# Kernel tuning notes

Hardware: AMD Instinct MI355X
Metric: run time of the kernel (lower is better)

Reference implementation:

```python
import jax, jax.numpy as jnp
import numpy as np
import math

NH = 12
EPS = 1e-7
BUCKET = 32
MAX_POS = 512

def make_position_indices(seq_len=MAX_POS, bucket_size=BUCKET, max_position=MAX_POS):
    rel = np.arange(max_position)[:, None] - np.arange(max_position)[None, :]
    sign = np.sign(rel)
    mid = bucket_size // 2
    abs_pos = np.where((rel < mid) & (rel > -mid), mid - 1, np.abs(rel)).astype(np.float64)
    log_pos = np.ceil(np.log(abs_pos / mid) / math.log((max_position - 1) / mid) * (mid - 1)).astype(np.int64) + mid
    bucket_pos = np.where(abs_pos <= mid, rel, log_pos * sign).astype(np.int64)
    idx = (bucket_size - 1 + bucket_pos).astype(np.int32)
    return idx[:seq_len, :seq_len]

def setup_inputs() -> dict:
    key = jax.random.key(0)
    S, B, H, I, L = 512, 8, 768, 2048, 6
    ks = jax.random.split(key, 16)
    std = math.sqrt(2.0 / (5.0 * H))
    inp = {
        'hidden_states': jax.random.normal(ks[0], (S, B, H), jnp.float32),
        'attention_mask': jnp.zeros((B, 1, 1, S), dtype=bool),
        'relative_embedding': jax.random.normal(ks[1], (2 * BUCKET - 1, H), jnp.float32) * 0.02,
        'Wqk': jax.random.normal(ks[2], (L, 2 * H, H), jnp.float32) * std,
        'bqk': jnp.zeros((L, 2 * H), jnp.float32),
        'Wv': jax.random.normal(ks[3], (L, H, H), jnp.float32) * std,
        'bv': jnp.zeros((L, H), jnp.float32),
        'Wo': jax.random.normal(ks[4], (L, H, H), jnp.float32) * std,
        'bo': jnp.zeros((L, H), jnp.float32),
        'ln_g': jnp.ones((L, H), jnp.float32),
        'ln_b': jnp.zeros((L, H), jnp.float32),
        'W1': jax.random.normal(ks[5], (L, 2 * I, H), jnp.float32) * std,
        'W2': jax.random.normal(ks[6], (L, H, I), jnp.float32) * std,
        'position_indices': jnp.asarray(make_position_indices(S)),
    }
    return inp

def _ln(x):
    mu = jnp.mean(x, axis=-1, keepdims=True)
    xc = x - mu
    var = jnp.mean(xc * xc, axis=-1, keepdims=True)
    return xc / jnp.sqrt(var + EPS)

def _encoder(hidden_states, attention_mask, relative_embedding, Wqk, bqk, Wv, bv, Wo, bo, ln_g, ln_b, W1, W2, position_indices):
    S, B, H = hidden_states.shape
    hd = H // NH
    scale = 1.0 / math.sqrt(3 * hd)
    mask = attention_mask  # bool [B,1,1,S], True = masked out

    def layer(x, p):
        Wqk_, bqk_, Wv_, bv_, Wo_, bo_, g_, b_, W1_, W2_ = p
        h = _ln(x)  # pre-LN, no affine
        qk = h @ Wqk_.T + bqk_            # [S,B,2H]
        q, k = jnp.split(qk, 2, axis=-1)
        v = h @ Wv_.T + bv_               # [S,B,H]
        # relative position projections
        pos = relative_embedding @ Wqk_.T + bqk_          # [R,2H]
        pos = pos[position_indices]                        # [S,S,2H]
        pos = pos.reshape(S, S, NH, 2 * hd)
        qpos, kpos = pos[..., :hd], pos[..., hd:]          # [S,S,NH,hd]
        q = q.reshape(S, B, NH, hd).transpose(1, 2, 0, 3)  # [B,NH,S,hd]
        k = k.reshape(S, B, NH, hd).transpose(1, 2, 0, 3)
        v = v.reshape(S, B, NH, hd).transpose(1, 2, 0, 3)
        scores = jnp.einsum('bhqd,bhkd->bhqk', q, k) * scale
        scores = scores + jnp.einsum('bhqd,qkhd->bhqk', q, kpos) * scale
        scores = scores + jnp.einsum('bhkd,qkhd->bhqk', k, qpos) * scale
        scores = jnp.where(mask, -jnp.inf, scores)
        probs = jax.nn.softmax(scores, axis=-1)
        probs = jnp.where(mask, 0.0, probs)
        ctx = jnp.einsum('bhqk,bhkd->bhqd', probs, v)      # [B,NH,S,hd]
        ctx = ctx.transpose(2, 0, 1, 3).reshape(S, B, H)
        ctx = ctx @ Wo_.T + bo_
        ctx = _ln(ctx) * g_ + b_                            # post-LN with affine
        x = x + ctx
        # GeGLU FFN
        h = _ln(x)
        u = h @ W1_.T                                       # [S,B,2I]
        a, gate = jnp.split(u, 2, axis=-1)
        u = a * jax.nn.gelu(gate, approximate=True)
        u = _ln(u)
        u = u @ W2_.T
        x = x + u
        return x, None

    x, _ = jax.lax.scan(layer, hidden_states, (Wqk, bqk, Wv, bv, Wo, bo, ln_g, ln_b, W1, W2))
    return x

def reference(hidden_states, attention_mask, relative_embedding, Wqk, bqk, Wv, bv, Wo, bo, ln_g, ln_b, W1, W2, position_indices):
    return _encoder(hidden_states, attention_mask, relative_embedding, Wqk, bqk, Wv, bv, Wo, bo, ln_g, ln_b, W1, W2, position_indices)
```

## Files before the change

### kernel.cpp

```cpp
#include <hip/hip_runtime.h>
#include <math.h>

typedef unsigned short u16;
typedef unsigned int u32;
typedef short bf16x8 __attribute__((ext_vector_type(8)));
typedef float f32x4 __attribute__((ext_vector_type(4)));

__device__ __forceinline__ float bf2f(u16 b) {
    u32 x = ((u32)b) << 16;
    return __builtin_bit_cast(float, x);
}
__device__ __forceinline__ u16 f2bf(float f) {
    u32 u = __builtin_bit_cast(u32, f);
    u32 r = (u + 0x7fffu + ((u >> 16) & 1u)) >> 16;
    return (u16)r;
}
__device__ __forceinline__ float wave_red_sum(float v) {
#pragma unroll
    for (int o = 32; o; o >>= 1) v += __shfl_down(v, o, 64);
    return v;
}


__global__ void convert_kernel(const float* __restrict__ in, u16* __restrict__ out, int n) {
    for (int i = blockIdx.x * 256 + threadIdx.x; i < n; i += gridDim.x * 256)
        out[i] = f2bf(in[i]);
}

__global__ void copy_kernel(const float* __restrict__ in, float* __restrict__ out, int n) {
    for (int i = blockIdx.x * 256 + threadIdx.x; i < n; i += gridDim.x * 256)
        out[i] = in[i];
}

__global__ void relpad_kernel(const float* __restrict__ rel, u16* __restrict__ relpad) {
    int i = blockIdx.x * 256 + threadIdx.x;
    if (i >= 64 * 768) return;
    relpad[i] = (i < 63 * 768) ? f2bf(rel[i]) : (u16)0;
}

__global__ void diag_kernel(unsigned char* __restrict__ diag8) {
    int i = blockIdx.x * 256 + threadIdx.x;
    if (i >= 1023) return;
    int rel = i - 511;
    int sgn = (rel > 0) - (rel < 0);
    int arel = rel < 0 ? -rel : rel;
    double abs_pos = (rel < 16 && rel > -16) ? 15.0 : (double)arel;
    int bucket;
    if (abs_pos <= 16.0) {
        bucket = rel;
    } else {
        double lp = ceil(log(abs_pos / 16.0) / log(511.0 / 16.0) * 15.0);
        bucket = ((int)lp + 16) * sgn;
    }
    diag8[i] = (unsigned char)(31 + bucket);
}

__global__ __launch_bounds__(256) void ln_plain(const float* __restrict__ x, u16* __restrict__ h) {
    int m = blockIdx.x, t = threadIdx.x;
    const float* row = x + (size_t)m * 768;
    float v0 = row[t], v1 = row[t + 256], v2 = row[t + 512];
    __shared__ float red[4];
    float s = wave_red_sum(v0 + v1 + v2);
    if ((t & 63) == 0) red[t >> 6] = s;
    __syncthreads();
    float mean = (red[0] + red[1] + red[2] + red[3]) * (1.f / 768.f);
    __syncthreads();
    float d0 = v0 - mean, d1 = v1 - mean, d2 = v2 - mean;
    float q = wave_red_sum(d0 * d0 + d1 * d1 + d2 * d2);
    if ((t & 63) == 0) red[t >> 6] = q;
    __syncthreads();
    float inv = rsqrtf((red[0] + red[1] + red[2] + red[3]) * (1.f / 768.f) + 1e-7f);
    u16* hr = h + (size_t)m * 768;
    hr[t] = f2bf(d0 * inv);
    hr[t + 256] = f2bf(d1 * inv);
    hr[t + 512] = f2bf(d2 * inv);
}

__global__ __launch_bounds__(256) void ln_res(const float* __restrict__ c, const float* __restrict__ g,
                                              const float* __restrict__ bb, float* __restrict__ x) {
    int m = blockIdx.x, t = threadIdx.x;
    const float* row = c + (size_t)m * 768;
    float v0 = row[t], v1 = row[t + 256], v2 = row[t + 512];
    __shared__ float red[4];
    float s = wave_red_sum(v0 + v1 + v2);
    if ((t & 63) == 0) red[t >> 6] = s;
    __syncthreads();
    float mean = (red[0] + red[1] + red[2] + red[3]) * (1.f / 768.f);
    __syncthreads();
    float d0 = v0 - mean, d1 = v1 - mean, d2 = v2 - mean;
    float q = wave_red_sum(d0 * d0 + d1 * d1 + d2 * d2);
    if ((t & 63) == 0) red[t >> 6] = q;
    __syncthreads();
    float inv = rsqrtf((red[0] + red[1] + red[2] + red[3]) * (1.f / 768.f) + 1e-7f);
    float* xr = x + (size_t)m * 768;
    xr[t] += d0 * inv * g[t] + bb[t];
    xr[t + 256] += d1 * inv * g[t + 256] + bb[t + 256];
    xr[t + 512] += d2 * inv * g[t + 512] + bb[t + 512];
}

__device__ __forceinline__ float fast_tanh(float z) {
    return 1.f - 2.f / (__expf(2.f * z) + 1.f);
}

__global__ __launch_bounds__(256) void glu_ln(const u16* __restrict__ u, u16* __restrict__ h2) {
    int m = blockIdx.x, t = threadIdx.x;
    const u16* row = u + (size_t)m * 4096;
    float gv[8];
    float s = 0.f;
#pragma unroll
    for (int jj = 0; jj < 8; jj++) {
        int j = jj * 256 + t;
        float a = bf2f(row[j]);
        float gt = bf2f(row[2048 + j]);
        float ge = 0.5f * gt * (1.f + fast_tanh(0.7978845608028654f * (gt + 0.044715f * gt * gt * gt)));
        gv[jj] = a * ge;
        s += gv[jj];
    }
    __shared__ float red[4];
    s = wave_red_sum(s);
    if ((t & 63) == 0) red[t >> 6] = s;
    __syncthreads();
    float mean = (red[0] + red[1] + red[2] + red[3]) * (1.f / 2048.f);
    __syncthreads();
    float q2 = 0.f;
#pragma unroll
    for (int jj = 0; jj < 8; jj++) {
        float d = gv[jj] - mean;
        q2 += d * d;
    }
    q2 = wave_red_sum(q2);
    if ((t & 63) == 0) red[t >> 6] = q2;
    __syncthreads();
    float inv = rsqrtf((red[0] + red[1] + red[2] + red[3]) * (1.f / 2048.f) + 1e-7f);
    u16* out = h2 + (size_t)m * 2048;
#pragma unroll
    for (int jj = 0; jj < 8; jj++) out[jj * 256 + t] = f2bf((gv[jj] - mean) * inv);
}

__global__ __launch_bounds__(256) void gemm_nt(const u16* __restrict__ A, const u16* __restrict__ B,
                                               const float* __restrict__ bias, int M, int N, int K,
                                               int mode, void* __restrict__ out0, void* __restrict__ out1) {
    __shared__ __align__(16) u16 As[128 * 72];
    __shared__ __align__(16) u16 Bs[128 * 72];
    const int t = threadIdx.x;
    const int lane = t & 63, wave = t >> 6;
    const int wm = (wave >> 1) * 64, wn = (wave & 1) * 64;
    const int fr = lane & 15, qd = lane >> 4;
    const int m0 = blockIdx.y * 128, n0 = blockIdx.x * 128;
    const int row_s = t >> 3, g_s = t & 7;

    f32x4 zero4 = {0.f, 0.f, 0.f, 0.f};
    f32x4 acc[4][4];
#pragma unroll
    for (int i = 0; i < 4; i++)
#pragma unroll
        for (int j = 0; j < 4; j++) acc[i][j] = zero4;

    for (int k0 = 0; k0 < K; k0 += 64) {
        __syncthreads();
#pragma unroll
        for (int it = 0; it < 4; ++it) {
            int row = it * 32 + row_s;
            const float4* src = (const float4*)(A + (size_t)(m0 + row) * K + k0 + g_s * 8);
            *(float4*)&As[row * 72 + g_s * 8] = *src;
        }
#pragma unroll
        for (int it = 0; it < 4; ++it) {
            int row = it * 32 + row_s;
            const float4* src = (const float4*)(B + (size_t)(n0 + row) * K + k0 + g_s * 8);
            *(float4*)&Bs[row * 72 + g_s * 8] = *src;
        }
        __syncthreads();
#pragma unroll
        for (int s = 0; s < 2; ++s) {
            bf16x8 aF[4], bF[4];
#pragma unroll
            for (int i = 0; i < 4; i++) aF[i] = *(const bf16x8*)&As[(wm + i * 16 + fr) * 72 + s * 32 + qd * 8];
#pragma unroll
            for (int j = 0; j < 4; j++) bF[j] = *(const bf16x8*)&Bs[(wn + j * 16 + fr) * 72 + s * 32 + qd * 8];
#pragma unroll
            for (int i = 0; i < 4; i++)
#pragma unroll
                for (int j = 0; j < 4; j++)
                    acc[i][j] = __builtin_amdgcn_mfma_f32_16x16x32_bf16(aF[i], bF[j], acc[i][j], 0, 0, 0);
        }
    }

#pragma unroll
    for (int j = 0; j < 4; j++) {
        int nn = n0 + wn + j * 16 + fr;
        float bval = bias ? bias[nn] : 0.f;
#pragma unroll
        for (int i = 0; i < 4; i++) {
#pragma unroll
            for (int rg = 0; rg < 4; ++rg) {
                int mm = m0 + wm + i * 16 + qd * 4 + rg;
                float val = acc[i][j][rg] + bval;
                if (mode == 0) {
                    ((float*)out0)[(size_t)mm * N + nn] = val;
                } else if (mode == 1) {
                    ((u16*)out0)[(size_t)mm * N + nn] = f2bf(val);
                } else if (mode == 2) {
                    int sidx = mm >> 3, bidx = mm & 7;
                    int nn2 = nn;
                    u16* dst = (u16*)out0;
                    if (nn2 >= 768) { dst = (u16*)out1; nn2 -= 768; }
                    int hh = nn2 >> 6, dd = nn2 & 63;
                    dst[(size_t)((bidx * 12 + hh) * 512 + sidx) * 64 + dd] = f2bf(val);
                } else if (mode == 3) {
                    int sidx = mm >> 3, bidx = mm & 7;
                    int hh = nn >> 6, dd = nn & 63;
                    ((u16*)out0)[(size_t)((bidx * 12 + hh) * 64 + dd) * 512 + sidx] = f2bf(val);
                } else {
                    ((float*)out0)[(size_t)mm * N + nn] += val;
                }
            }
        }
    }
}


__global__ __launch_bounds__(256) void pos_mfma(const u16* __restrict__ relpad, const u16* __restrict__ wqk_all,
                                                const float* __restrict__ bqk_all, u16* __restrict__ qposb,
                                                u16* __restrict__ kposb) {
    __shared__ __align__(16) u16 As[64 * 72];
    __shared__ __align__(16) u16 Bs[64 * 72];
    int t = threadIdx.x, lane = t & 63, w = t >> 6;
    int fr = lane & 15, qd = lane >> 4;
    int n0 = blockIdx.x * 64, l = blockIdx.y;
    const u16* B = wqk_all + (size_t)l * 1536 * 768;
    const float* bias = bqk_all + (size_t)l * 1536;
    int rs = t >> 2, cs = (t & 3) * 16;
    f32x4 zero4 = {0.f, 0.f, 0.f, 0.f};
    f32x4 acc[4];
#pragma unroll
    for (int j = 0; j < 4; j++) acc[j] = zero4;

    for (int k0 = 0; k0 < 768; k0 += 64) {
        __syncthreads();
        const u16* ga = relpad + (size_t)rs * 768 + k0 + cs;
        *(float4*)&As[rs * 72 + cs] = *(const float4*)ga;
        *(float4*)&As[rs * 72 + cs + 8] = *(const float4*)(ga + 8);
        const u16* gb = B + (size_t)(n0 + rs) * 768 + k0 + cs;
        *(float4*)&Bs[rs * 72 + cs] = *(const float4*)gb;
        *(float4*)&Bs[rs * 72 + cs + 8] = *(const float4*)(gb + 8);
        __syncthreads();
#pragma unroll
        for (int s = 0; s < 2; s++) {
            bf16x8 aF = *(const bf16x8*)&As[(w * 16 + fr) * 72 + s * 32 + qd * 8];
#pragma unroll
            for (int jf = 0; jf < 4; jf++) {
                bf16x8 bF = *(const bf16x8*)&Bs[(jf * 16 + fr) * 72 + s * 32 + qd * 8];
                acc[jf] = __builtin_amdgcn_mfma_f32_16x16x32_bf16(aF, bF, acc[jf], 0, 0, 0);
            }
        }
    }
#pragma unroll
    for (int jf = 0; jf < 4; jf++) {
        int nn = n0 + jf * 16 + fr;
        float bval = bias[nn];
        int hh = nn >> 7, wd = nn & 127;
#pragma unroll
        for (int rg = 0; rg < 4; rg++) {
            int m = w * 16 + qd * 4 + rg;
            if (m >= 63) continue;
            float val = acc[jf][rg] + bval;
            size_t o = ((size_t)l * 12 + hh) * 64 * 64 + (size_t)m * 64;
            if (wd < 64) qposb[o + wd] = f2bf(val);
            else kposb[o + (wd - 64)] = f2bf(val);
        }
    }
}

__global__ __launch_bounds__(256) void posdot_kernel(const u16* __restrict__ qbuf, const u16* __restrict__ kbuf,
                                                     const u16* __restrict__ qposb, const u16* __restrict__ kposb,
                                                     u16* __restrict__ c2pb, u16* __restrict__ p2cb) {
    __shared__ __align__(16) u16 Qs[128 * 72];
    __shared__ __align__(16) u16 Ks[128 * 72];
    __shared__ __align__(16) u16 QP[64 * 72];
    __shared__ __align__(16) u16 KP[64 * 72];
    const float scale = 0.07216878364870323f;
    int t = threadIdx.x, lane = t & 63, w = t >> 6;
    int fr = lane & 15, qd = lane >> 4;
    int s0 = blockIdx.x * 128, bh = blockIdx.y, h = bh % 12;
    size_t base = (size_t)bh * 512 * 64;
    {
        int rs = t >> 1, cs = (t & 1) * 32;
#pragma unroll
        for (int c = 0; c < 4; c++) {
            *(float4*)&Qs[rs * 72 + cs + c * 8] = *(const float4*)(qbuf + base + (size_t)(s0 + rs) * 64 + cs + c * 8);
            *(float4*)&Ks[rs * 72 + cs + c * 8] = *(const float4*)(kbuf + base + (size_t)(s0 + rs) * 64 + cs + c * 8);
        }
        int rs2 = t >> 2, cs2 = (t & 3) * 16;
        const u16* qp = qposb + (size_t)h * 64 * 64;
        const u16* kp = kposb + (size_t)h * 64 * 64;
#pragma unroll
        for (int c = 0; c < 2; c++) {
            *(float4*)&QP[rs2 * 72 + cs2 + c * 8] = *(const float4*)(qp + (size_t)rs2 * 64 + cs2 + c * 8);
            *(float4*)&KP[rs2 * 72 + cs2 + c * 8] = *(const float4*)(kp + (size_t)rs2 * 64 + cs2 + c * 8);
        }
    }
    __syncthreads();
    f32x4 zero4 = {0.f, 0.f, 0.f, 0.f};
    f32x4 cacc[2][4], pacc[2][4];
#pragma unroll
    for (int i = 0; i < 2; i++)
#pragma unroll
        for (int j = 0; j < 4; j++) { cacc[i][j] = zero4; pacc[i][j] = zero4; }
#pragma unroll
    for (int s = 0; s < 2; s++) {
#pragma unroll
        for (int i = 0; i < 2; i++) {
            bf16x8 aQ = *(const bf16x8*)&Qs[(w * 32 + i * 16 + fr) * 72 + s * 32 + qd * 8];
            bf16x8 aK = *(const bf16x8*)&Ks[(w * 32 + i * 16 + fr) * 72 + s * 32 + qd * 8];
#pragma unroll
            for (int jf = 0; jf < 4; jf++) {
                bf16x8 bKP = *(const bf16x8*)&KP[(jf * 16 + fr) * 72 + s * 32 + qd * 8];
                bf16x8 bQP = *(const bf16x8*)&QP[(jf * 16 + fr) * 72 + s * 32 + qd * 8];
                cacc[i][jf] = __builtin_amdgcn_mfma_f32_16x16x32_bf16(aQ, bKP, cacc[i][jf], 0, 0, 0);
                pacc[i][jf] = __builtin_amdgcn_mfma_f32_16x16x32_bf16(aK, bQP, pacc[i][jf], 0, 0, 0);
            }
        }
    }
#pragma unroll
    for (int i = 0; i < 2; i++)
#pragma unroll
        for (int jf = 0; jf < 4; jf++)
#pragma unroll
            for (int rg = 0; rg < 4; rg++) {
                int row = w * 32 + i * 16 + qd * 4 + rg;
                int col = jf * 16 + fr;
                size_t o = (size_t)(bh * 512 + s0 + row) * 64 + col;
                c2pb[o] = f2bf(cacc[i][jf][rg] * scale);
                p2cb[o] = f2bf(pacc[i][jf][rg] * scale);
            }
}

__global__ __launch_bounds__(256) void attn_mfma(const u16* __restrict__ qbuf, const u16* __restrict__ kbuf,
                                                 const u16* __restrict__ vbT, const u16* __restrict__ c2pb,
                                                 const u16* __restrict__ p2cb, const unsigned char* __restrict__ diag8,
                                                 const unsigned char* __restrict__ mask, u16* __restrict__ ctxb) {
    __shared__ __align__(16) u16 Qs[64 * 72];
    __shared__ __align__(16) u16 KsPs[64 * 72];
    __shared__ __align__(16) u16 Vt[64 * 72];
    __shared__ __align__(16) u16 c2ps[64 * 72];
    __shared__ __align__(16) u16 p2cs[64 * 72];
    __shared__ unsigned char idxd[576];
    __shared__ unsigned char mks[512];
    const float scale = 0.07216878364870323f;
    int t = threadIdx.x, lane = t & 63, w = t >> 6;
    int fr = lane & 15, qd = lane >> 4;
    int qt = blockIdx.x, bh = blockIdx.y;
    int b = bh / 12, h = bh % 12;
    int q0 = qt * 64;
    size_t base = (size_t)bh * 512 * 64;
    int rs = t >> 2, cs = (t & 3) * 16;

    {
        const u16* gq = qbuf + base + (size_t)(q0 + rs) * 64 + cs;
        *(float4*)&Qs[rs * 72 + cs] = *(const float4*)gq;
        *(float4*)&Qs[rs * 72 + cs + 8] = *(const float4*)(gq + 8);
        const u16* gc = c2pb + (size_t)(bh * 512 + q0 + rs) * 64 + cs;
        *(float4*)&c2ps[rs * 72 + cs] = *(const float4*)gc;
        *(float4*)&c2ps[rs * 72 + cs + 8] = *(const float4*)(gc + 8);
        for (int i = t; i < 575; i += 256) idxd[i] = diag8[q0 + i];
        for (int i = t; i < 512; i += 256) mks[i] = mask[b * 512 + i];
    }

    f32x4 zero4 = {0.f, 0.f, 0.f, 0.f};
    f32x4 oacc[4];
#pragma unroll
    for (int j = 0; j < 4; j++) oacc[j] = zero4;
    float m_i[4] = {-1e30f, -1e30f, -1e30f, -1e30f};
    float l_i[4] = {0.f, 0.f, 0.f, 0.f};
    const int ql0 = w * 16 + qd * 4;

    for (int kt = 0; kt < 8; kt++) {
        __syncthreads();
        {
            const u16* gk = kbuf + base + (size_t)(kt * 64 + rs) * 64 + cs;
            *(float4*)&KsPs[rs * 72 + cs] = *(const float4*)gk;
            *(float4*)&KsPs[rs * 72 + cs + 8] = *(const float4*)(gk + 8);
            const u16* gv = vbT + base + (size_t)rs * 512 + kt * 64 + cs;
            *(float4*)&Vt[rs * 72 + cs] = *(const float4*)gv;
            *(float4*)&Vt[rs * 72 + cs + 8] = *(const float4*)(gv + 8);
            const u16* gp = p2cb + (size_t)(bh * 512 + kt * 64 + rs) * 64 + cs;
            *(float4*)&p2cs[rs * 72 + cs] = *(const float4*)gp;
            *(float4*)&p2cs[rs * 72 + cs + 8] = *(const float4*)(gp + 8);
        }
        __syncthreads();

        f32x4 sacc[4];
#pragma unroll
        for (int j = 0; j < 4; j++) sacc[j] = zero4;
#pragma unroll
        for (int s = 0; s < 2; s++) {
            bf16x8 aQ = *(const bf16x8*)&Qs[(w * 16 + fr) * 72 + s * 32 + qd * 8];
#pragma unroll
            for (int jf = 0; jf < 4; jf++) {
                bf16x8 bK = *(const bf16x8*)&KsPs[(jf * 16 + fr) * 72 + s * 32 + qd * 8];
                sacc[jf] = __builtin_amdgcn_mfma_f32_16x16x32_bf16(aQ, bK, sacc[jf], 0, 0, 0);
            }
        }

        float pvv[4][4];
#pragma unroll
        for (int jf = 0; jf < 4; jf++) {
            int kl = jf * 16 + fr;
            int kg = kt * 64 + kl;
            bool mk = mks[kg] != 0;
#pragma unroll
            for (int rg = 0; rg < 4; rg++) {
                int ql = ql0 + rg;
                int j = idxd[ql - kg + 511];
                float bias = bf2f(c2ps[ql * 72 + j]) + bf2f(p2cs[kl * 72 + j]);
                float sval = sacc[jf][rg] * scale + bias;
                pvv[jf][rg] = mk ? -1e30f : sval;
            }
        }

#pragma unroll
        for (int rg = 0; rg < 4; rg++) {
            float rm = fmaxf(fmaxf(pvv[0][rg], pvv[1][rg]), fmaxf(pvv[2][rg], pvv[3][rg]));
#pragma unroll
            for (int msk = 1; msk < 16; msk <<= 1) rm = fmaxf(rm, __shfl_xor(rm, msk));
            float mnew = fmaxf(m_i[rg], rm);
            float alpha = __expf(m_i[rg] - mnew);
            m_i[rg] = mnew;
            float rsum = 0.f;
#pragma unroll
            for (int jf = 0; jf < 4; jf++) {
                float p = __expf(pvv[jf][rg] - mnew);
                pvv[jf][rg] = p;
                rsum += p;
            }
#pragma unroll
            for (int msk = 1; msk < 16; msk <<= 1) rsum += __shfl_xor(rsum, msk);
            l_i[rg] = l_i[rg] * alpha + rsum;
#pragma unroll
            for (int jf = 0; jf < 4; jf++) oacc[jf][rg] *= alpha;
        }

        __syncthreads();

        u16* Psw = &KsPs[w * 16 * 72];
#pragma unroll
        for (int jf = 0; jf < 4; jf++)
#pragma unroll
            for (int rg = 0; rg < 4; rg++) Psw[(qd * 4 + rg) * 72 + jf * 16 + fr] = f2bf(pvv[jf][rg]);

#pragma unroll
        for (int s = 0; s < 2; s++) {
            bf16x8 aP = *(const bf16x8*)&Psw[fr * 72 + s * 32 + qd * 8];
#pragma unroll
            for (int jf = 0; jf < 4; jf++) {
                bf16x8 bV = *(const bf16x8*)&Vt[(jf * 16 + fr) * 72 + s * 32 + qd * 8];
                oacc[jf] = __builtin_amdgcn_mfma_f32_16x16x32_bf16(aP, bV, oacc[jf], 0, 0, 0);
            }
        }
    }

#pragma unroll
    for (int jf = 0; jf < 4; jf++) {
#pragma unroll
        for (int rg = 0; rg < 4; rg++) {
            int qg = q0 + ql0 + rg;
            int d = jf * 16 + fr;
            float o = oacc[jf][rg] / l_i[rg];
            int m = qg * 8 + b;
            ctxb[(size_t)m * 768 + h * 64 + d] = f2bf(o);
        }
    }
}


extern "C" void kernel_launch(void* const* d_in, const int* in_sizes, int n_in, void* d_out, int out_size,
                              void* d_ws, size_t ws_size, hipStream_t stream) {
    const float* hidden = (const float*)d_in[0];
    const unsigned char* mask = (const unsigned char*)d_in[1];
    const float* relemb = (const float*)d_in[2];
    const float* Wqk = (const float*)d_in[3];
    const float* bqk = (const float*)d_in[4];
    const float* Wv = (const float*)d_in[5];
    const float* bv = (const float*)d_in[6];
    const float* Wo = (const float*)d_in[7];
    const float* bo = (const float*)d_in[8];
    const float* lng = (const float*)d_in[9];
    const float* lnb = (const float*)d_in[10];
    const float* W1 = (const float*)d_in[11];
    const float* W2 = (const float*)d_in[12];
    float* x = (float*)d_out;

    char* wsp = (char*)d_ws;
    auto alloc = [&](size_t bytes) -> char* {
        char* p = wsp;
        wsp += (bytes + 255) & ~(size_t)255;
        return p;
    };
    u16* wqk_bf = (u16*)alloc(6ull * 1536 * 768 * 2);
    u16* wv_bf = (u16*)alloc(6ull * 768 * 768 * 2);
    u16* wo_bf = (u16*)alloc(6ull * 768 * 768 * 2);
    u16* w1_bf = (u16*)alloc(6ull * 4096 * 768 * 2);
    u16* w2_bf = (u16*)alloc(6ull * 768 * 2048 * 2);
    u16* h_bf = (u16*)alloc(4096ull * 768 * 2);
    u16* qb = (u16*)alloc(96ull * 512 * 64 * 2);
    u16* kb = (u16*)alloc(96ull * 512 * 64 * 2);
    u16* vbT = (u16*)alloc(96ull * 512 * 64 * 2);
    u16* qposb = (u16*)alloc(6ull * 12 * 64 * 64 * 2);
    u16* kposb = (u16*)alloc(6ull * 12 * 64 * 64 * 2);
    u16* relpad = (u16*)alloc(64ull * 768 * 2);
    u16* c2pb = (u16*)alloc(96ull * 512 * 64 * 2);
    u16* p2cb = (u16*)alloc(96ull * 512 * 64 * 2);
    unsigned char* diag8 = (unsigned char*)alloc(1024);
    u16* ctxb = (u16*)alloc(4096ull * 768 * 2);
    float* ctxproj = (float*)alloc(4096ull * 768 * 4);
    u16* ubuf = (u16*)alloc(4096ull * 4096 * 2);
    u16* h2 = (u16*)alloc(4096ull * 2048 * 2);
    (void)ws_size;
    (void)in_sizes;
    (void)n_in;
    (void)out_size;

    auto conv = [&](const float* in, u16* out, size_t n) {
        size_t blocks = (n + 255) / 256;
        if (blocks > 8192) blocks = 8192;
        convert_kernel<<<dim3((unsigned)blocks), dim3(256), 0, stream>>>(in, out, (int)n);
    };
    conv(Wqk, wqk_bf, 6ull * 1536 * 768);
    conv(Wv, wv_bf, 6ull * 768 * 768);
    conv(Wo, wo_bf, 6ull * 768 * 768);
    conv(W1, w1_bf, 6ull * 4096 * 768);
    conv(W2, w2_bf, 6ull * 768 * 2048);
    copy_kernel<<<dim3(4096), dim3(256), 0, stream>>>(hidden, x, 4096 * 768);
    diag_kernel<<<dim3(4), dim3(256), 0, stream>>>(diag8);
    relpad_kernel<<<dim3(192), dim3(256), 0, stream>>>(relemb, relpad);
    pos_mfma<<<dim3(24, 6), dim3(256), 0, stream>>>(relpad, wqk_bf, bqk, qposb, kposb);

    for (int l = 0; l < 6; l++) {
        ln_plain<<<dim3(4096), dim3(256), 0, stream>>>(x, h_bf);
        gemm_nt<<<dim3(12, 32), dim3(256), 0, stream>>>(h_bf, wqk_bf + (size_t)l * 1536 * 768, bqk + l * 1536,
                                                        4096, 1536, 768, 2, qb, kb);
        gemm_nt<<<dim3(6, 32), dim3(256), 0, stream>>>(h_bf, wv_bf + (size_t)l * 768 * 768, bv + l * 768,
                                                       4096, 768, 768, 3, vbT, nullptr);
        posdot_kernel<<<dim3(4, 96), dim3(256), 0, stream>>>(qb, kb, qposb + (size_t)l * 12 * 64 * 64,
                                                             kposb + (size_t)l * 12 * 64 * 64, c2pb, p2cb);
        attn_mfma<<<dim3(8, 96), dim3(256), 0, stream>>>(qb, kb, vbT, c2pb, p2cb, diag8, mask, ctxb);
        gemm_nt<<<dim3(6, 32), dim3(256), 0, stream>>>(ctxb, wo_bf + (size_t)l * 768 * 768, bo + l * 768,
                                                       4096, 768, 768, 0, ctxproj, nullptr);
        ln_res<<<dim3(4096), dim3(256), 0, stream>>>(ctxproj, lng + l * 768, lnb + l * 768, x);
        ln_plain<<<dim3(4096), dim3(256), 0, stream>>>(x, h_bf);
        gemm_nt<<<dim3(32, 32), dim3(256), 0, stream>>>(h_bf, w1_bf + (size_t)l * 4096 * 768, nullptr,
                                                        4096, 4096, 768, 1, ubuf, nullptr);
        glu_ln<<<dim3(4096), dim3(256), 0, stream>>>(ubuf, h2);
        gemm_nt<<<dim3(6, 32), dim3(256), 0, stream>>>(h2, w2_bf + (size_t)l * 768 * 2048, nullptr,
                                                       4096, 768, 2048, 4, x, nullptr);
    }
}
```

Measured before the change: 1.861 ms.

## Fuse QKV projection GEMMs and use 64x64 tiles for narrow N=768 GEMMs

The Wqk and Wv weights and biases are concatenated into one [2304,768] matrix per layer, so the Q/K and V projections run as a single GEMM whose epilogue scatters into the q, k and transposed v layouts. The output-projection and FFN down-projection GEMMs (N=768) move to a new 64x64-tile kernel with a grid of 768 blocks instead of 192, which fills more compute units on the device, plus an XCD-aware block-index remap. The smaller tiles give less data reuse per block, and the fused epilogue adds a branch per element.

Measured after the change: 1.658 ms. -10.9%, faster.

```diff
diff --git a/kernel.cpp b/kernel.cpp
--- a/kernel.cpp
+++ b/kernel.cpp
@@ -25,6 +25,26 @@
 __global__ void convert_kernel(const float* __restrict__ in, u16* __restrict__ out, int n) {
     for (int i = blockIdx.x * 256 + threadIdx.x; i < n; i += gridDim.x * 256)
         out[i] = f2bf(in[i]);
+}
+
+__global__ void convert_qkv_kernel(const float* __restrict__ Wqk, const float* __restrict__ Wv,
+                                   u16* __restrict__ out) {
+    const int per = 2304 * 768;
+    for (int i = blockIdx.x * 256 + threadIdx.x; i < 6 * per; i += gridDim.x * 256) {
+        int l = i / per, r = i % per;
+        int row = r / 768, col = r % 768;
+        float v = (row < 1536) ? Wqk[((size_t)l * 1536 + row) * 768 + col]
+                               : Wv[((size_t)l * 768 + (row - 1536)) * 768 + col];
+        out[i] = f2bf(v);
+    }
+}
+
+__global__ void bias_qkv_kernel(const float* __restrict__ bqk, const float* __restrict__ bv,
+                                float* __restrict__ out) {
+    for (int i = blockIdx.x * 256 + threadIdx.x; i < 6 * 2304; i += gridDim.x * 256) {
+        int l = i / 2304, r = i % 2304;
+        out[i] = (r < 1536) ? bqk[l * 1536 + r] : bv[l * 768 + (r - 1536)];
+    }
 }
 
 __global__ void copy_kernel(const float* __restrict__ in, float* __restrict__ out, int n) {
@@ -139,7 +159,8 @@
 
 __global__ __launch_bounds__(256) void gemm_nt(const u16* __restrict__ A, const u16* __restrict__ B,
                                                const float* __restrict__ bias, int M, int N, int K,
-                                               int mode, void* __restrict__ out0, void* __restrict__ out1) {
+                                               int mode, void* __restrict__ out0, void* __restrict__ out1,
+                                               void* __restrict__ out2) {
     __shared__ __align__(16) u16 As[128 * 72];
     __shared__ __align__(16) u16 Bs[128 * 72];
     const int t = threadIdx.x;
@@ -196,40 +217,106 @@
             for (int rg = 0; rg < 4; ++rg) {
                 int mm = m0 + wm + i * 16 + qd * 4 + rg;
                 float val = acc[i][j][rg] + bval;
-                if (mode == 0) {
-                    ((float*)out0)[(size_t)mm * N + nn] = val;
-                } else if (mode == 1) {
+                if (mode == 1) {
                     ((u16*)out0)[(size_t)mm * N + nn] = f2bf(val);
-                } else if (mode == 2) {
+                } else {
                     int sidx = mm >> 3, bidx = mm & 7;
-                    int nn2 = nn;
-                    u16* dst = (u16*)out0;
-                    if (nn2 >= 768) { dst = (u16*)out1; nn2 -= 768; }
-                    int hh = nn2 >> 6, dd = nn2 & 63;
-                    dst[(size_t)((bidx * 12 + hh) * 512 + sidx) * 64 + dd] = f2bf(val);
-                } else if (mode == 3) {
-                    int sidx = mm >> 3, bidx = mm & 7;
-                    int hh = nn >> 6, dd = nn & 63;
-                    ((u16*)out0)[(size_t)((bidx * 12 + hh) * 64 + dd) * 512 + sidx] = f2bf(val);
-                } else {
-                    ((float*)out0)[(size_t)mm * N + nn] += val;
+                    if (nn < 1536) {
+                        int nn2 = nn;
+                        u16* dst = (u16*)out0;
+                        if (nn2 >= 768) { dst = (u16*)out1; nn2 -= 768; }
+                        int hh = nn2 >> 6, dd = nn2 & 63;
+                        dst[(size_t)((bidx * 12 + hh) * 512 + sidx) * 64 + dd] = f2bf(val);
+                    } else {
+                        int nn2 = nn - 1536;
+                        int hh = nn2 >> 6, dd = nn2 & 63;
+                        ((u16*)out2)[(size_t)((bidx * 12 + hh) * 64 + dd) * 512 + sidx] = f2bf(val);
+                    }
                 }
             }
         }
     }
 }
 
-
-__global__ __launch_bounds__(256) void pos_mfma(const u16* __restrict__ relpad, const u16* __restrict__ wqk_all,
-                                                const float* __restrict__ bqk_all, u16* __restrict__ qposb,
+__global__ __launch_bounds__(256) void gemm64(const u16* __restrict__ A, const u16* __restrict__ B,
+                                              const float* __restrict__ bias, int M, int N, int K,
+                                              int mode, float* __restrict__ out) {
+    __shared__ __align__(16) u16 As[64 * 72];
+    __shared__ __align__(16) u16 Bs[64 * 72];
+    const int t = threadIdx.x;
+    const int lane = t & 63, w = t >> 6;
+    const int wm = (w >> 1) * 32, wn = (w & 1) * 32;
+    const int fr = lane & 15, qd = lane >> 4;
+    const int nt = N >> 6, mt = M >> 6;
+    int lin = blockIdx.x;
+    int c = lin & 7, s = lin >> 3;
+    int m0 = (c * (mt >> 3) + s / nt) * 64;
+    int n0 = (s % nt) * 64;
+    const int rs = t >> 2, cs = (t & 3) * 16;
+
+    f32x4 zero4 = {0.f, 0.f, 0.f, 0.f};
+    f32x4 acc[2][2];
+#pragma unroll
+    for (int i = 0; i < 2; i++)
+#pragma unroll
+        for (int j = 0; j < 2; j++) acc[i][j] = zero4;
+
+    for (int k0 = 0; k0 < K; k0 += 64) {
+        __syncthreads();
+        {
+            const u16* ga = A + (size_t)(m0 + rs) * K + k0 + cs;
+            *(float4*)&As[rs * 72 + cs] = *(const float4*)ga;
+            *(float4*)&As[rs * 72 + cs + 8] = *(const float4*)(ga + 8);
+            const u16* gb = B + (size_t)(n0 + rs) * K + k0 + cs;
+            *(float4*)&Bs[rs * 72 + cs] = *(const float4*)gb;
+            *(float4*)&Bs[rs * 72 + cs + 8] = *(const float4*)(gb + 8);
+        }
+        __syncthreads();
+#pragma unroll
+        for (int s2 = 0; s2 < 2; ++s2) {
+            bf16x8 aF[2], bF[2];
+#pragma unroll
+            for (int i = 0; i < 2; i++) aF[i] = *(const bf16x8*)&As[(wm + i * 16 + fr) * 72 + s2 * 32 + qd * 8];
+#pragma unroll
+            for (int j = 0; j < 2; j++) bF[j] = *(const bf16x8*)&Bs[(wn + j * 16 + fr) * 72 + s2 * 32 + qd * 8];
+#pragma unroll
+            for (int i = 0; i < 2; i++)
+#pragma unroll
+                for (int j = 0; j < 2; j++)
+                    acc[i][j] = __builtin_amdgcn_mfma_f32_16x16x32_bf16(aF[i], bF[j], acc[i][j], 0, 0, 0);
+        }
+    }
+
+#pragma unroll
+    for (int j = 0; j < 2; j++) {
+        int nn = n0 + wn + j * 16 + fr;
+        float bval = bias ? bias[nn] : 0.f;
+#pragma unroll
+        for (int i = 0; i < 2; i++) {
+#pragma unroll
+            for (int rg = 0; rg < 4; ++rg) {
+                int mm = m0 + wm + i * 16 + qd * 4 + rg;
+                float val = acc[i][j][rg] + bval;
+                if (mode == 0)
+                    out[(size_t)mm * N + nn] = val;
+                else
+                    out[(size_t)mm * N + nn] += val;
+            }
+        }
+    }
+}
+
+
+__global__ __launch_bounds__(256) void pos_mfma(const u16* __restrict__ relpad, const u16* __restrict__ wqkv_all,
+                                                const float* __restrict__ bqkv_all, u16* __restrict__ qposb,
                                                 u16* __restrict__ kposb) {
     __shared__ __align__(16) u16 As[64 * 72];
     __shared__ __align__(16) u16 Bs[64 * 72];
     int t = threadIdx.x, lane = t & 63, w = t >> 6;
     int fr = lane & 15, qd = lane >> 4;
     int n0 = blockIdx.x * 64, l = blockIdx.y;
-    const u16* B = wqk_all + (size_t)l * 1536 * 768;
-    const float* bias = bqk_all + (size_t)l * 1536;
+    const u16* B = wqkv_all + (size_t)l * 2304 * 768;
+    const float* bias = bqkv_all + (size_t)l * 2304;
     int rs = t >> 2, cs = (t & 3) * 16;
     f32x4 zero4 = {0.f, 0.f, 0.f, 0.f};
     f32x4 acc[4];
@@ -497,8 +584,8 @@
         wsp += (bytes + 255) & ~(size_t)255;
         return p;
     };
-    u16* wqk_bf = (u16*)alloc(6ull * 1536 * 768 * 2);
-    u16* wv_bf = (u16*)alloc(6ull * 768 * 768 * 2);
+    u16* wqkv_bf = (u16*)alloc(6ull * 2304 * 768 * 2);
+    float* bqkv = (float*)alloc(6ull * 2304 * 4);
     u16* wo_bf = (u16*)alloc(6ull * 768 * 768 * 2);
     u16* w1_bf = (u16*)alloc(6ull * 4096 * 768 * 2);
     u16* w2_bf = (u16*)alloc(6ull * 768 * 2048 * 2);
@@ -526,33 +613,31 @@
         if (blocks > 8192) blocks = 8192;
         convert_kernel<<<dim3((unsigned)blocks), dim3(256), 0, stream>>>(in, out, (int)n);
     };
-    conv(Wqk, wqk_bf, 6ull * 1536 * 768);
-    conv(Wv, wv_bf, 6ull * 768 * 768);
+    convert_qkv_kernel<<<dim3(8192), dim3(256), 0, stream>>>(Wqk, Wv, wqkv_bf);
+    bias_qkv_kernel<<<dim3(54), dim3(256), 0, stream>>>(bqk, bv, bqkv);
     conv(Wo, wo_bf, 6ull * 768 * 768);
     conv(W1, w1_bf, 6ull * 4096 * 768);
     conv(W2, w2_bf, 6ull * 768 * 2048);
     copy_kernel<<<dim3(4096), dim3(256), 0, stream>>>(hidden, x, 4096 * 768);
     diag_kernel<<<dim3(4), dim3(256), 0, stream>>>(diag8);
     relpad_kernel<<<dim3(192), dim3(256), 0, stream>>>(relemb, relpad);
-    pos_mfma<<<dim3(24, 6), dim3(256), 0, stream>>>(relpad, wqk_bf, bqk, qposb, kposb);
+    pos_mfma<<<dim3(24, 6), dim3(256), 0, stream>>>(relpad, wqkv_bf, bqkv, qposb, kposb);
 
     for (int l = 0; l < 6; l++) {
         ln_plain<<<dim3(4096), dim3(256), 0, stream>>>(x, h_bf);
-        gemm_nt<<<dim3(12, 32), dim3(256), 0, stream>>>(h_bf, wqk_bf + (size_t)l * 1536 * 768, bqk + l * 1536,
-                                                        4096, 1536, 768, 2, qb, kb);
-        gemm_nt<<<dim3(6, 32), dim3(256), 0, stream>>>(h_bf, wv_bf + (size_t)l * 768 * 768, bv + l * 768,
-                                                       4096, 768, 768, 3, vbT, nullptr);
+        gemm_nt<<<dim3(18, 32), dim3(256), 0, stream>>>(h_bf, wqkv_bf + (size_t)l * 2304 * 768, bqkv + l * 2304,
+                                                        4096, 2304, 768, 5, qb, kb, vbT);
         posdot_kernel<<<dim3(4, 96), dim3(256), 0, stream>>>(qb, kb, qposb + (size_t)l * 12 * 64 * 64,
                                                              kposb + (size_t)l * 12 * 64 * 64, c2pb, p2cb);
         attn_mfma<<<dim3(8, 96), dim3(256), 0, stream>>>(qb, kb, vbT, c2pb, p2cb, diag8, mask, ctxb);
-        gemm_nt<<<dim3(6, 32), dim3(256), 0, stream>>>(ctxb, wo_bf + (size_t)l * 768 * 768, bo + l * 768,
-                                                       4096, 768, 768, 0, ctxproj, nullptr);
+        gemm64<<<dim3(768), dim3(256), 0, stream>>>(ctxb, wo_bf + (size_t)l * 768 * 768, bo + l * 768,
+                                                    4096, 768, 768, 0, ctxproj);
         ln_res<<<dim3(4096), dim3(256), 0, stream>>>(ctxproj, lng + l * 768, lnb + l * 768, x);
         ln_plain<<<dim3(4096), dim3(256), 0, stream>>>(x, h_bf);
         gemm_nt<<<dim3(32, 32), dim3(256), 0, stream>>>(h_bf, w1_bf + (size_t)l * 4096 * 768, nullptr,
-                                                        4096, 4096, 768, 1, ubuf, nullptr);
+                                                        4096, 4096, 768, 1, ubuf, nullptr, nullptr);
         glu_ln<<<dim3(4096), dim3(256), 0, stream>>>(ubuf, h2);
-        gemm_nt<<<dim3(6, 32), dim3(256), 0, stream>>>(h2, w2_bf + (size_t)l * 768 * 2048, nullptr,
-                                                       4096, 768, 2048, 4, x, nullptr);
-    }
-}
+        gemm64<<<dim3(768), dim3(256), 0, stream>>>(h2, w2_bf + (size_t)l * 768 * 2048, nullptr,
+                                                    4096, 768, 2048, 4, x);
+    }
+}
```
